# Kernel tuning notes

Hardware: AMD Instinct MI355X
Metric: run time of the kernel (lower is better)

The kernel has to match this reference:

```python
import jax, jax.numpy as jnp
import numpy as np

N_NODES = 150000
N_EDGES = 300000
N_LG_EDGES = 600000
N_TREE = 60000
HIDDEN = 256
DEPTH = 4
ATOM_FDIM = 35
BOND_FDIM = 5
NUM_GRAPHS = 2048


def setup_inputs() -> dict:
    key = jax.random.key(0)
    ks = jax.random.split(key, 14)
    return {
        "node_x": jax.random.normal(ks[0], (N_NODES, ATOM_FDIM), dtype=jnp.float32),
        "bond_x": jax.random.normal(ks[1], (N_EDGES, BOND_FDIM), dtype=jnp.float32),
        "tree_mess": jax.random.normal(ks[2], (N_TREE, HIDDEN), dtype=jnp.float32),
        "W_i": jax.random.normal(ks[3], (ATOM_FDIM + BOND_FDIM, HIDDEN), dtype=jnp.float32) * 0.05,
        "W_h": jax.random.normal(ks[4], (HIDDEN, HIDDEN), dtype=jnp.float32) * 0.05,
        "W_o": jax.random.normal(ks[5], (ATOM_FDIM + HIDDEN, HIDDEN), dtype=jnp.float32) * 0.05,
        "b_o": jax.random.normal(ks[6], (HIDDEN,), dtype=jnp.float32) * 0.05,
        "edge_src": jax.random.randint(ks[7], (N_EDGES,), 0, N_NODES, dtype=jnp.int64 if jax.config.jax_enable_x64 else jnp.int32).astype(jnp.int32),
        "edge_dst": jax.random.randint(ks[8], (N_EDGES,), 0, N_NODES).astype(jnp.int32),
        "lg_src": jax.random.randint(ks[9], (N_LG_EDGES,), 0, N_EDGES).astype(jnp.int32),
        "lg_dst": jax.random.randint(ks[10], (N_LG_EDGES,), 0, N_EDGES).astype(jnp.int32),
        "tgt_nodes": jax.random.randint(ks[11], (N_TREE,), 0, N_NODES).astype(jnp.int32),
        "graph_ids": jnp.sort(jax.random.randint(ks[12], (N_NODES,), 0, NUM_GRAPHS)).astype(jnp.int32),
        "num_graphs": NUM_GRAPHS,
    }


def reference(node_x, bond_x, tree_mess, W_i, W_h, W_o, b_o,
              edge_src, edge_dst, lg_src, lg_dst, tgt_nodes, graph_ids, num_graphs):
    n_nodes = node_x.shape[0]
    n_edges = bond_x.shape[0]

    # msg_input = W_i([src_atom_x ; bond_x])  (no bias)
    features = jnp.concatenate([node_x[edge_src], bond_x], axis=1)  # [E, 40]
    msg_input = features @ W_i                                       # [E, H]
    msg = jax.nn.relu(msg_input)

    # tree-message alpha: scatter_add tree messages onto target atoms (non-PAPER branch)
    node_alpha = jnp.zeros((n_nodes, msg.shape[1]), msg.dtype).at[tgt_nodes].add(tree_mess)
    edge_alpha = node_alpha[edge_src]  # apply_edges: alpha = src['alpha']

    # loopy BP on the line graph: accum = sum of incoming line-graph messages
    def body(msg, _):
        accum = jax.ops.segment_sum(msg[lg_src], lg_dst, num_segments=n_edges)
        msg = jax.nn.relu(msg_input + (accum + edge_alpha) @ W_h)
        return msg, None

    msg, _ = jax.lax.scan(body, msg, None, length=DEPTH - 1)

    # gather: m[v] = sum of msg over incoming edges; h = relu(W_o([x ; m + alpha]) + b)
    m = jax.ops.segment_sum(msg, edge_dst, num_segments=n_nodes)
    h = jax.nn.relu(jnp.concatenate([node_x, m + node_alpha], axis=1) @ W_o + b_o)

    # mean_nodes per graph
    counts = jax.ops.segment_sum(jnp.ones((n_nodes,), h.dtype), graph_ids, num_segments=num_graphs)
    g_sum = jax.ops.segment_sum(h, graph_ids, num_segments=num_graphs)
    g_repr = g_sum / jnp.maximum(counts, 1.0)[:, None]
    return g_repr
```

## Files before the change

### kernel.cpp

```cpp
#include <hip/hip_runtime.h>
#include <stdint.h>

#define HID 256
#define CAP 16

typedef __attribute__((ext_vector_type(8))) short bf16x8;
typedef __attribute__((ext_vector_type(4))) float f32x4;
typedef __attribute__((ext_vector_type(2))) float f32x2;

__device__ __forceinline__ float bf2f(unsigned short u) {
    union { unsigned int i; float f; } v; v.i = ((unsigned int)u) << 16; return v.f;
}
__device__ __forceinline__ unsigned short f2bf(float f) {
    union { float f; unsigned int i; } v; v.f = f;
    unsigned int r = (v.i + 0x7fffu + ((v.i >> 16) & 1u)) >> 16;
    return (unsigned short)r;
}
__device__ __forceinline__ float fp82f_sw(unsigned char b) {
    unsigned int s = (unsigned int)(b & 0x80) << 24;
    int e = (b >> 3) & 0xF;
    int m = b & 7;
    float v;
    if (e) v = __uint_as_float(((unsigned int)(e + 120) << 23) | ((unsigned int)m << 20));
    else   v = (float)m * 0.001953125f;
    return __uint_as_float(__float_as_uint(v) | s);
}
__device__ __forceinline__ unsigned char f2fp8_sw(float x) {
    unsigned int bits = __float_as_uint(x);
    unsigned char s = (unsigned char)((bits >> 24) & 0x80);
    float ax = fabsf(x);
    if (!(ax >= 0.001953125f)) {
        int n = (int)rintf(ax * 512.f);
        return s | (unsigned char)n;
    }
    if (ax >= 448.f) return s | 0x7E;
    int ex; float mant = frexpf(ax, &ex);
    int e = ex + 6;
    if (e >= 1) {
        int q = (int)rintf(mant * 16.f);
        if (q == 16) { q = 8; ++e; }
        if (e > 15 || (e == 15 && q > 14)) return s | 0x7E;
        return s | (unsigned char)((e << 3) | (q - 8));
    } else {
        int n = (int)rintf(ax * 512.f);
        if (n >= 8) return s | 0x08;
        return s | (unsigned char)n;
    }
}
__device__ __forceinline__ unsigned char f2fp8(float x) {
#if __has_builtin(__builtin_amdgcn_cvt_pk_fp8_f32)
    return (unsigned char)(__builtin_amdgcn_cvt_pk_fp8_f32(x, x, 0, false) & 0xff);
#else
    return f2fp8_sw(x);
#endif
}
__device__ __forceinline__ f32x4 fp8x4_to_f32(unsigned int u) {
#if __has_builtin(__builtin_amdgcn_cvt_pk_f32_fp8)
    f32x2 a = __builtin_amdgcn_cvt_pk_f32_fp8(u, false);
    f32x2 b = __builtin_amdgcn_cvt_pk_f32_fp8(u, true);
    f32x4 r; r[0] = a.x; r[1] = a.y; r[2] = b.x; r[3] = b.y;
    return r;
#else
    f32x4 r;
    #pragma unroll
    for (int q = 0; q < 4; ++q) r[q] = fp82f_sw((u >> (8 * q)) & 0xff);
    return r;
#endif
}
__device__ __forceinline__ bf16x8 fp8x8_to_bf16x8(uint2 raw) {
#if __has_builtin(__builtin_amdgcn_cvt_pk_f32_fp8)
    f32x2 p0 = __builtin_amdgcn_cvt_pk_f32_fp8(raw.x, false);
    f32x2 p1 = __builtin_amdgcn_cvt_pk_f32_fp8(raw.x, true);
    f32x2 p2 = __builtin_amdgcn_cvt_pk_f32_fp8(raw.y, false);
    f32x2 p3 = __builtin_amdgcn_cvt_pk_f32_fp8(raw.y, true);
    union { unsigned int u[4]; bf16x8 v; } cv;
    cv.u[0] = (__float_as_uint(p0.x) >> 16) | (__float_as_uint(p0.y) & 0xffff0000u);
    cv.u[1] = (__float_as_uint(p1.x) >> 16) | (__float_as_uint(p1.y) & 0xffff0000u);
    cv.u[2] = (__float_as_uint(p2.x) >> 16) | (__float_as_uint(p2.y) & 0xffff0000u);
    cv.u[3] = (__float_as_uint(p3.x) >> 16) | (__float_as_uint(p3.y) & 0xffff0000u);
    return cv.v;
#else
    union { unsigned short u[8]; bf16x8 v; } cv;
    #pragma unroll
    for (int q = 0; q < 4; ++q) cv.u[q]     = f2bf(fp82f_sw((raw.x >> (8 * q)) & 0xff));
    #pragma unroll
    for (int q = 0; q < 4; ++q) cv.u[4 + q] = f2bf(fp82f_sw((raw.y >> (8 * q)) & 0xff));
    return cv.v;
#endif
}

__device__ __forceinline__ void llds16(const void* g, void* l) {
    __builtin_amdgcn_global_load_lds(
        (const __attribute__((address_space(1))) void*)g,
        (__attribute__((address_space(3))) void*)l, 16, 0, 0);
}


__global__ void k_zero_f(float* __restrict__ p, size_t n) {
    size_t i = (size_t)blockIdx.x * 256 + threadIdx.x;
    if (i < n) p[i] = 0.f;
}
__global__ void k_diag(float* __restrict__ out, float v) {
    if (blockIdx.x == 0 && threadIdx.x == 0) out[0] = v;
}

__global__ void k_init(int* __restrict__ cnt_lg, int E,
                       int* __restrict__ cnt_nd, int* __restrict__ cnt_t, int N,
                       int* __restrict__ gcnt, int* __restrict__ gstart, int G) {
    int i = blockIdx.x * 256 + threadIdx.x;
    if (i < E) cnt_lg[i] = 0;
    if (i < N) { cnt_nd[i] = 0; cnt_t[i] = 0; }
    if (i < G) { gcnt[i] = 0; gstart[i] = N; }
}

__global__ void k_alpha(const float* __restrict__ tm, const int* __restrict__ cnt,
                        const int* __restrict__ bkt, unsigned char* __restrict__ alpha, int N) {
    int wave = threadIdx.x >> 6, lane = threadIdx.x & 63;
    int v = blockIdx.x * 4 + wave;
    if (v >= N) return;
    int d = cnt[v]; if (d > CAP) d = CAP;
    f32x4 s = {0.f, 0.f, 0.f, 0.f};
    const int* bb = bkt + (size_t)v * CAP;
    for (int t = 0; t < d; ++t) {
        int r = bb[t];
        f32x4 x = *(const f32x4*)(tm + (size_t)r * HID + lane * 4);
        #pragma unroll
        for (int k = 0; k < 4; ++k) s[k] += x[k];
    }
    union { unsigned char b[4]; unsigned int u; } ov;
    #pragma unroll
    for (int k = 0; k < 4; ++k) ov.b[k] = f2fp8(s[k]);
    *(unsigned int*)(alpha + (size_t)v * HID + lane * 4) = ov.u;
}

__global__ void k_wt_i(const float* __restrict__ W, unsigned short* __restrict__ Wt) {
    int i = blockIdx.x * 256 + threadIdx.x;
    int n = i >> 6, k = i & 63;
    Wt[i] = f2bf((k < 40) ? W[k * HID + n] : 0.f);
}
__global__ void k_wt_hi(const float* __restrict__ Wh, const float* __restrict__ Wi,
                        unsigned short* __restrict__ Wt) {
    int i = blockIdx.x * 256 + threadIdx.x;
    int n = i / 320, k = i % 320;
    float v;
    if (k < 256) v = Wh[(size_t)k * HID + n];
    else if (k < 296) v = Wi[(size_t)(k - 256) * HID + n];
    else v = 0.f;
    Wt[i] = f2bf(v);
}
__global__ void k_wt_o(const float* __restrict__ W, unsigned short* __restrict__ Wt) {
    int i = blockIdx.x * 256 + threadIdx.x;
    int n = i / 320, k = i % 320;
    float v;
    if (k < 256) v = W[(size_t)(35 + k) * HID + n];
    else if (k < 291) v = W[(size_t)(k - 256) * HID + n];
    else v = 0.f;
    Wt[i] = f2bf(v);
}

__global__ void k_a1(const float* __restrict__ nx, const float* __restrict__ bx,
                     const int* __restrict__ esrc, unsigned char* __restrict__ A1, int E) {
    int i = blockIdx.x * 256 + threadIdx.x;
    if (i >= E * 64) return;
    int e = i >> 6, k = i & 63;
    float v = 0.f;
    if (k < 35) v = nx[(size_t)esrc[e] * 35 + k];
    else if (k < 40) v = bx[(size_t)e * 5 + (k - 35)];
    A1[i] = f2fp8(v);
}

__global__ void k_x1(const float* __restrict__ nx, unsigned char* __restrict__ X1, int N) {
    int i = blockIdx.x * 256 + threadIdx.x;
    if (i >= N * 64) return;
    int v = i >> 6, k = i & 63;
    X1[i] = f2fp8((k < 35) ? nx[(size_t)v * 35 + k] : 0.f);
}

__global__ void k_fill(const int* __restrict__ dst, const int* __restrict__ val,
                       int* __restrict__ cnt, int* __restrict__ bkt, int n, int useval) {
    int i = blockIdx.x * 256 + threadIdx.x;
    if (i >= n) return;
    int d = dst[i];
    int p = atomicAdd(&cnt[d], 1);
    if (p < CAP) bkt[(size_t)d * CAP + p] = useval ? val[i] : i;
}

__global__ void k_gfill(const int* __restrict__ gid, int* __restrict__ gstart,
                        int* __restrict__ gcnt, int N) {
    int i = blockIdx.x * 256 + threadIdx.x;
    if (i >= N) return;
    int g = gid[i];
    atomicAdd(&gcnt[g], 1);
    atomicMin(&gstart[g], i);
}

template<int K1, int KTOT, int EPI, bool PF8, bool QF8, bool OUTF8>
__global__ __launch_bounds__(256, 2)
void gemm4(const void* __restrict__ Ap, int lda1,
           const void* __restrict__ Aq, int lda2,
           const unsigned short* __restrict__ B, int M,
           void* __restrict__ out, const float* __restrict__ bias)
{
    constexpr int NKC = KTOT / 64;
    __shared__ unsigned char Als[128 * 128];
    __shared__ unsigned char Bls[256 * 128];
    const int tid  = threadIdx.x;
    const int lane = tid & 63;
    const int wid  = tid >> 6;
    const int wm = wid & 1, wn = wid >> 1;
    const int row0 = blockIdx.x * 128;
    const int l15  = lane & 15;
    const int quad = lane >> 4;

    f32x4 acc[4][8] = {};

    const int sA8_r = lane >> 2, sA8_c = lane & 3;
    const int s16_r = lane >> 3, s16_c = lane & 7;

    #pragma unroll
    for (int kc = 0; kc < NKC; ++kc) {
        const bool pPart = (kc * 64 < K1);
        const void* As = pPart ? Ap : Aq;
        const int  lda  = pPart ? lda1 : lda2;
        const int  kofs = pPart ? kc * 64 : kc * 64 - K1;
        const bool f8   = pPart ? PF8 : QF8;

        if (f8) {
            #pragma unroll
            for (int t = 0; t < 2; ++t) {
                int r = wid * 32 + t * 16 + sA8_r;
                int ar = row0 + r; if (ar > M - 1) ar = M - 1;
                int ck = sA8_c ^ (r & 3);
                const unsigned char* g = (const unsigned char*)As + (size_t)ar * lda + kofs + ck * 16;
                llds16(g, &Als[(wid * 32 + t * 16) * 64]);
            }
        } else {
            #pragma unroll
            for (int t = 0; t < 4; ++t) {
                int r = wid * 32 + t * 8 + s16_r;
                int ar = row0 + r; if (ar > M - 1) ar = M - 1;
                int ck = s16_c ^ (r & 7);
                const unsigned char* g = (const unsigned char*)As + ((size_t)ar * lda + kofs) * 2 + ck * 16;
                llds16(g, &Als[(wid * 32 + t * 8) * 128]);
            }
        }
        #pragma unroll
        for (int t = 0; t < 8; ++t) {
            int r = wid * 64 + t * 8 + s16_r;
            int ck = s16_c ^ (r & 7);
            const unsigned char* g = (const unsigned char*)B + ((size_t)r * KTOT + kc * 64) * 2 + ck * 16;
            llds16(g, &Bls[(wid * 64 + t * 8) * 128]);
        }
        __syncthreads();

        #pragma unroll
        for (int kk = 0; kk < 64; kk += 32) {
            bf16x8 af[4];
            #pragma unroll
            for (int i = 0; i < 4; ++i) {
                int arow = wm * 64 + i * 16 + l15;
                if (f8) {
                    int ck = (kk >> 4) + (quad >> 1);
                    uint2 raw = *(const uint2*)&Als[arow * 64 + ((ck ^ (arow & 3)) << 4) + ((quad & 1) << 3)];
                    af[i] = fp8x8_to_bf16x8(raw);
                } else {
                    int ck = (kk >> 3) + quad;
                    af[i] = *(const bf16x8*)&Als[arow * 128 + ((ck ^ (arow & 7)) << 4)];
                }
            }
            #pragma unroll
            for (int j = 0; j < 8; ++j) {
                int brow = wn * 128 + j * 16 + l15;
                int ck = (kk >> 3) + quad;
                bf16x8 bfr = *(const bf16x8*)&Bls[brow * 128 + ((ck ^ (brow & 7)) << 4)];
                #pragma unroll
                for (int i = 0; i < 4; ++i)
                    acc[i][j] = __builtin_amdgcn_mfma_f32_16x16x32_bf16(af[i], bfr, acc[i][j], 0, 0, 0);
            }
        }
        if (kc + 1 < NKC) __syncthreads();
    }

    #pragma unroll
    for (int i = 0; i < 4; ++i) {
        int rbase = row0 + wm * 64 + i * 16 + quad * 4;
        #pragma unroll
        for (int r = 0; r < 4; ++r) {
            int row = rbase + r;
            if (row >= M) continue;
            #pragma unroll
            for (int j = 0; j < 8; ++j) {
                int col = wn * 128 + j * 16 + l15;
                float v = acc[i][j][r];
                if (EPI == 1) v += bias[col];
                v = v > 0.f ? v : 0.f;
                if (OUTF8) ((unsigned char*)out)[(size_t)row * HID + col] = f2fp8(v);
                else       ((unsigned short*)out)[(size_t)row * HID + col] = f2bf(v);
            }
        }
    }
}


__global__ void k_accum(const unsigned char* __restrict__ msg, const unsigned char* __restrict__ alpha,
                        const int* __restrict__ esrc, const int* __restrict__ cnt,
                        const int* __restrict__ bkt, unsigned char* __restrict__ accum, int E)
{
    int wave = threadIdx.x >> 6;
    int lane = threadIdx.x & 63;
    int sub  = lane >> 5;
    int sl   = lane & 31;
    int e = blockIdx.x * 8 + wave * 2 + sub;
    if (e >= E) return;
    int c = sl * 8;
    int src = esrc[e];
    int d = cnt[e]; if (d > CAP) d = CAP;
    uint2 au = *(const uint2*)(alpha + (size_t)src * HID + c);
    f32x4 s0 = fp8x4_to_f32(au.x);
    f32x4 s1 = fp8x4_to_f32(au.y);
    const int* bb = bkt + (size_t)e * CAP;
    for (int base = 0; base < d; base += 4) {
        int4 bi = *(const int4*)(bb + base);
        int rem = d - base;
        int i0 = bi.x;
        int i1 = (rem > 1) ? bi.y : bi.x;
        int i2 = (rem > 2) ? bi.z : bi.x;
        int i3 = (rem > 3) ? bi.w : bi.x;
        uint2 m0 = *(const uint2*)(msg + (size_t)i0 * HID + c);
        uint2 m1 = *(const uint2*)(msg + (size_t)i1 * HID + c);
        uint2 m2 = *(const uint2*)(msg + (size_t)i2 * HID + c);
        uint2 m3 = *(const uint2*)(msg + (size_t)i3 * HID + c);
        {   f32x4 vx = fp8x4_to_f32(m0.x), vy = fp8x4_to_f32(m0.y);
            #pragma unroll
            for (int k = 0; k < 4; ++k) { s0[k] += vx[k]; s1[k] += vy[k]; } }
        if (rem > 1) { f32x4 vx = fp8x4_to_f32(m1.x), vy = fp8x4_to_f32(m1.y);
            #pragma unroll
            for (int k = 0; k < 4; ++k) { s0[k] += vx[k]; s1[k] += vy[k]; } }
        if (rem > 2) { f32x4 vx = fp8x4_to_f32(m2.x), vy = fp8x4_to_f32(m2.y);
            #pragma unroll
            for (int k = 0; k < 4; ++k) { s0[k] += vx[k]; s1[k] += vy[k]; } }
        if (rem > 3) { f32x4 vx = fp8x4_to_f32(m3.x), vy = fp8x4_to_f32(m3.y);
            #pragma unroll
            for (int k = 0; k < 4; ++k) { s0[k] += vx[k]; s1[k] += vy[k]; } }
    }
    union { unsigned char b[8]; uint2 u; } ov;
    #pragma unroll
    for (int k = 0; k < 4; ++k) { ov.b[k] = f2fp8(s0[k]); ov.b[4 + k] = f2fp8(s1[k]); }
    *(uint2*)(accum + (size_t)e * HID + c) = ov.u;
}

__global__ void k_mpa(const unsigned char* __restrict__ msg, const unsigned char* __restrict__ alpha,
                      const int* __restrict__ cnt, const int* __restrict__ bkt,
                      unsigned short* __restrict__ Mb, int N)
{
    int wave = threadIdx.x >> 6;
    int lane = threadIdx.x & 63;
    int sub  = lane >> 5;
    int sl   = lane & 31;
    int v = blockIdx.x * 8 + wave * 2 + sub;
    if (v >= N) return;
    int c = sl * 8;
    int d = cnt[v]; if (d > CAP) d = CAP;
    uint2 au = *(const uint2*)(alpha + (size_t)v * HID + c);
    f32x4 s0 = fp8x4_to_f32(au.x);
    f32x4 s1 = fp8x4_to_f32(au.y);
    const int* bb = bkt + (size_t)v * CAP;
    for (int base = 0; base < d; base += 4) {
        int4 bi = *(const int4*)(bb + base);
        int rem = d - base;
        int i0 = bi.x;
        int i1 = (rem > 1) ? bi.y : bi.x;
        int i2 = (rem > 2) ? bi.z : bi.x;
        int i3 = (rem > 3) ? bi.w : bi.x;
        uint2 m0 = *(const uint2*)(msg + (size_t)i0 * HID + c);
        uint2 m1 = *(const uint2*)(msg + (size_t)i1 * HID + c);
        uint2 m2 = *(const uint2*)(msg + (size_t)i2 * HID + c);
        uint2 m3 = *(const uint2*)(msg + (size_t)i3 * HID + c);
        {   f32x4 vx = fp8x4_to_f32(m0.x), vy = fp8x4_to_f32(m0.y);
            #pragma unroll
            for (int k = 0; k < 4; ++k) { s0[k] += vx[k]; s1[k] += vy[k]; } }
        if (rem > 1) { f32x4 vx = fp8x4_to_f32(m1.x), vy = fp8x4_to_f32(m1.y);
            #pragma unroll
            for (int k = 0; k < 4; ++k) { s0[k] += vx[k]; s1[k] += vy[k]; } }
        if (rem > 2) { f32x4 vx = fp8x4_to_f32(m2.x), vy = fp8x4_to_f32(m2.y);
            #pragma unroll
            for (int k = 0; k < 4; ++k) { s0[k] += vx[k]; s1[k] += vy[k]; } }
        if (rem > 3) { f32x4 vx = fp8x4_to_f32(m3.x), vy = fp8x4_to_f32(m3.y);
            #pragma unroll
            for (int k = 0; k < 4; ++k) { s0[k] += vx[k]; s1[k] += vy[k]; } }
    }
    union { unsigned short h[8]; uint4 u; } ov;
    #pragma unroll
    for (int k = 0; k < 4; ++k) { ov.h[k] = f2bf(s0[k]); ov.h[4 + k] = f2bf(s1[k]); }
    *(uint4*)(Mb + (size_t)v * HID + c) = ov.u;
}

__global__ void k_gmean(const unsigned short* __restrict__ h, const int* __restrict__ gstart,
                        const int* __restrict__ gcnt, float* __restrict__ out, int G) {
    int g = blockIdx.x;
    int c = threadIdx.x;
    int st = gstart[g], n = gcnt[g];
    float s = 0.f;
    for (int r = 0; r < n; ++r) s += bf2f(h[(size_t)(st + r) * HID + c]);
    out[(size_t)g * HID + c] = (n > 0) ? s / (float)n : 0.f;
}

extern "C" void kernel_launch(void* const* d_in, const int* in_sizes, int n_in,
                              void* d_out, int out_size, void* d_ws, size_t ws_size,
                              hipStream_t stream)
{
    const float* node_x    = (const float*)d_in[0];
    const float* bond_x    = (const float*)d_in[1];
    const float* tree_mess = (const float*)d_in[2];
    const float* W_i       = (const float*)d_in[3];
    const float* W_h       = (const float*)d_in[4];
    const float* W_o       = (const float*)d_in[5];
    const float* b_o       = (const float*)d_in[6];
    const int* edge_src    = (const int*)d_in[7];
    const int* edge_dst    = (const int*)d_in[8];
    const int* lg_src      = (const int*)d_in[9];
    const int* lg_dst      = (const int*)d_in[10];
    const int* tgt_nodes   = (const int*)d_in[11];
    const int* graph_ids   = (const int*)d_in[12];

    const int N = in_sizes[0] / 35;
    const int E = in_sizes[1] / 5;
    const int T = in_sizes[2] / HID;
    const int L = in_sizes[9];
    const int G = out_size / HID;

    auto rup = [](size_t b) { return (b + 255) & ~(size_t)255; };
    const size_t szAcc = (size_t)E * HID;
    const size_t szMsg = (size_t)E * HID;
    const size_t szMbN = (size_t)N * HID * 2;
    const size_t R_acc = rup(szAcc > szMbN ? szAcc : szMbN);
    const size_t R_msg = rup(szMsg > szMbN ? szMsg : szMbN);
    const size_t R_al  = rup((size_t)N * HID);
    const size_t R_a1  = rup((size_t)E * 64);
    const size_t need = R_acc + R_msg + R_al + R_a1
        + rup(256 * 64 * 2) + rup((size_t)256 * 320 * 2) * 2
        + rup((size_t)E * 4) + rup((size_t)E * CAP * 4)
        + rup((size_t)N * 4) + rup((size_t)N * CAP * 4)
        + rup((size_t)N * 4) + rup((size_t)N * CAP * 4)
        + rup((size_t)G * 4) * 2;

    if (need > ws_size) {
        k_zero_f<<<(out_size + 255) / 256, 256, 0, stream>>>((float*)d_out, (size_t)out_size);
        k_diag<<<1, 64, 0, stream>>>((float*)d_out, (float)(ws_size >> 20));
        return;
    }

    char* w = (char*)d_ws;
    auto alloc = [&](size_t bytes) { char* p = w; w += (bytes + 255) & ~(size_t)255; return p; };
    char* r_acc = (char*)alloc(R_acc);
    char* r_msg = (char*)alloc(R_msg);
    char* r_al  = (char*)alloc(R_al);
    char* r_a1  = (char*)alloc(R_a1);
    unsigned short* Wt_i  = (unsigned short*)alloc(256 * 64 * 2);
    unsigned short* Wt_hi = (unsigned short*)alloc((size_t)256 * 320 * 2);
    unsigned short* Wt_o  = (unsigned short*)alloc((size_t)256 * 320 * 2);
    int* cnt_lg = (int*)alloc((size_t)E * 4);
    int* bkt_lg = (int*)alloc((size_t)E * CAP * 4);
    int* cnt_nd = (int*)alloc((size_t)N * 4);
    int* bkt_nd = (int*)alloc((size_t)N * CAP * 4);
    int* cnt_t  = (int*)alloc((size_t)N * 4);
    int* bkt_t  = (int*)alloc((size_t)N * CAP * 4);
    int* gstart = (int*)alloc((size_t)G * 4);
    int* gcnt   = (int*)alloc((size_t)G * 4);

    unsigned char*  accum = (unsigned char*)r_acc;
    unsigned short* Mb    = (unsigned short*)r_acc;
    unsigned char*  msg   = (unsigned char*)r_msg;
    unsigned short* h     = (unsigned short*)r_msg;
    unsigned char*  alpha = (unsigned char*)r_al;
    unsigned char*  A1    = (unsigned char*)r_a1;
    unsigned char*  X1    = (unsigned char*)r_a1;

    k_init<<<(E + 255) / 256, 256, 0, stream>>>(cnt_lg, E, cnt_nd, cnt_t, N, gcnt, gstart, G);

    k_wt_i<<<64, 256, 0, stream>>>(W_i, Wt_i);
    k_wt_hi<<<320, 256, 0, stream>>>(W_h, W_i, Wt_hi);
    k_wt_o<<<320, 256, 0, stream>>>(W_o, Wt_o);
    k_fill<<<(L + 255) / 256, 256, 0, stream>>>(lg_dst, lg_src, cnt_lg, bkt_lg, L, 1);
    k_fill<<<(E + 255) / 256, 256, 0, stream>>>(edge_dst, (const int*)nullptr, cnt_nd, bkt_nd, E, 0);
    k_fill<<<(T + 255) / 256, 256, 0, stream>>>(tgt_nodes, (const int*)nullptr, cnt_t, bkt_t, T, 0);
    k_gfill<<<(N + 255) / 256, 256, 0, stream>>>(graph_ids, gstart, gcnt, N);
    k_alpha<<<(N + 3) / 4, 256, 0, stream>>>(tree_mess, cnt_t, bkt_t, alpha, N);
    k_a1<<<(E * 64 + 255) / 256, 256, 0, stream>>>(node_x, bond_x, edge_src, A1, E);

    dim3 gE((E + 127) / 128, 1), gN((N + 127) / 128, 1);

    gemm4<0, 64, 0, false, true, true><<<gE, 256, 0, stream>>>(nullptr, 0, A1, 64, Wt_i, E, msg, nullptr);

    for (int it = 0; it < 3; ++it) {
        k_accum<<<(E + 7) / 8, 256, 0, stream>>>(msg, alpha, edge_src, cnt_lg, bkt_lg, accum, E);
        gemm4<256, 320, 0, true, true, true><<<gE, 256, 0, stream>>>(accum, 256, A1, 64, Wt_hi, E, msg, nullptr);
    }

    k_x1<<<(N * 64 + 255) / 256, 256, 0, stream>>>(node_x, X1, N);
    k_mpa<<<(N + 7) / 8, 256, 0, stream>>>(msg, alpha, cnt_nd, bkt_nd, Mb, N);
    gemm4<256, 320, 1, false, true, false><<<gN, 256, 0, stream>>>(Mb, 256, X1, 64, Wt_o, N, h, b_o);
    k_gmean<<<G, 256, 0, stream>>>(h, gstart, gcnt, (float*)d_out, G);
}
```

Measured before the change: 897.3 us.

## Double-buffer GEMM LDS staging, split output GEMM columns, widen accum vectors

Result: faster. 868.7 us (-3.2%).

```diff
diff --git a/kernel.cpp b/kernel.cpp
--- a/kernel.cpp
+++ b/kernel.cpp
@@ -194,37 +194,41 @@
     atomicMin(&gstart[g], i);
 }
 
-template<int K1, int KTOT, int EPI, bool PF8, bool QF8, bool OUTF8>
+template<int BN, int K1, int KTOT, int EPI, bool PF8, bool QF8, bool OUTF8>
 __global__ __launch_bounds__(256, 2)
-void gemm4(const void* __restrict__ Ap, int lda1,
+void gemm5(const void* __restrict__ Ap, int lda1,
            const void* __restrict__ Aq, int lda2,
            const unsigned short* __restrict__ B, int M,
            void* __restrict__ out, const float* __restrict__ bias)
 {
     constexpr int NKC = KTOT / 64;
-    __shared__ unsigned char Als[128 * 128];
-    __shared__ unsigned char Bls[256 * 128];
+    constexpr int NB  = (NKC > 1) ? 2 : 1;
+    constexpr bool ABF = (K1 > 0 && !PF8) || (KTOT > K1 && !QF8);
+    constexpr int ASZ = ABF ? 128 * 128 : 128 * 64;
+    constexpr int BSZ = BN * 128;
+    constexpr int JN  = BN / 32;
+    __shared__ unsigned char Als[NB * ASZ];
+    __shared__ unsigned char Bls[NB * BSZ];
     const int tid  = threadIdx.x;
     const int lane = tid & 63;
     const int wid  = tid >> 6;
     const int wm = wid & 1, wn = wid >> 1;
     const int row0 = blockIdx.x * 128;
+    const int colb = blockIdx.y * BN;
     const int l15  = lane & 15;
     const int quad = lane >> 4;
 
-    f32x4 acc[4][8] = {};
+    f32x4 acc[4][JN] = {};
 
     const int sA8_r = lane >> 2, sA8_c = lane & 3;
     const int s16_r = lane >> 3, s16_c = lane & 7;
 
-    #pragma unroll
-    for (int kc = 0; kc < NKC; ++kc) {
+    auto stageA = [&](int kc, int bb) {
         const bool pPart = (kc * 64 < K1);
         const void* As = pPart ? Ap : Aq;
         const int  lda  = pPart ? lda1 : lda2;
         const int  kofs = pPart ? kc * 64 : kc * 64 - K1;
         const bool f8   = pPart ? PF8 : QF8;
-
         if (f8) {
             #pragma unroll
             for (int t = 0; t < 2; ++t) {
@@ -232,7 +236,7 @@
                 int ar = row0 + r; if (ar > M - 1) ar = M - 1;
                 int ck = sA8_c ^ (r & 3);
                 const unsigned char* g = (const unsigned char*)As + (size_t)ar * lda + kofs + ck * 16;
-                llds16(g, &Als[(wid * 32 + t * 16) * 64]);
+                llds16(g, &Als[bb + (wid * 32 + t * 16) * 64]);
             }
         } else {
             #pragma unroll
@@ -241,18 +245,29 @@
                 int ar = row0 + r; if (ar > M - 1) ar = M - 1;
                 int ck = s16_c ^ (r & 7);
                 const unsigned char* g = (const unsigned char*)As + ((size_t)ar * lda + kofs) * 2 + ck * 16;
-                llds16(g, &Als[(wid * 32 + t * 8) * 128]);
+                llds16(g, &Als[bb + (wid * 32 + t * 8) * 128]);
             }
         }
+    };
+    auto stageB = [&](int kc, int bb) {
         #pragma unroll
-        for (int t = 0; t < 8; ++t) {
-            int r = wid * 64 + t * 8 + s16_r;
+        for (int t = 0; t < BN / 32; ++t) {
+            int r = wid * (BN / 4) + t * 8 + s16_r;
             int ck = s16_c ^ (r & 7);
-            const unsigned char* g = (const unsigned char*)B + ((size_t)r * KTOT + kc * 64) * 2 + ck * 16;
-            llds16(g, &Bls[(wid * 64 + t * 8) * 128]);
+            const unsigned char* g = (const unsigned char*)B + ((size_t)(colb + r) * KTOT + kc * 64) * 2 + ck * 16;
+            llds16(g, &Bls[bb + (wid * (BN / 4) + t * 8) * 128]);
         }
+    };
+
+    stageA(0, 0);
+    stageB(0, 0);
+    int cur = 0;
+    #pragma unroll
+    for (int kc = 0; kc < NKC; ++kc) {
         __syncthreads();
-
+        if (kc + 1 < NKC) { stageA(kc + 1, (cur ^ 1) * ASZ); stageB(kc + 1, (cur ^ 1) * BSZ); }
+        const bool f8 = (kc * 64 < K1) ? PF8 : QF8;
+        const int abase = cur * ASZ, bbase = cur * BSZ;
         #pragma unroll
         for (int kk = 0; kk < 64; kk += 32) {
             bf16x8 af[4];
@@ -261,24 +276,24 @@
                 int arow = wm * 64 + i * 16 + l15;
                 if (f8) {
                     int ck = (kk >> 4) + (quad >> 1);
-                    uint2 raw = *(const uint2*)&Als[arow * 64 + ((ck ^ (arow & 3)) << 4) + ((quad & 1) << 3)];
+                    uint2 raw = *(const uint2*)&Als[abase + arow * 64 + ((ck ^ (arow & 3)) << 4) + ((quad & 1) << 3)];
                     af[i] = fp8x8_to_bf16x8(raw);
                 } else {
                     int ck = (kk >> 3) + quad;
-                    af[i] = *(const bf16x8*)&Als[arow * 128 + ((ck ^ (arow & 7)) << 4)];
+                    af[i] = *(const bf16x8*)&Als[abase + arow * 128 + ((ck ^ (arow & 7)) << 4)];
                 }
             }
             #pragma unroll
-            for (int j = 0; j < 8; ++j) {
-                int brow = wn * 128 + j * 16 + l15;
+            for (int j = 0; j < JN; ++j) {
+                int brow = wn * (BN / 2) + j * 16 + l15;
                 int ck = (kk >> 3) + quad;
-                bf16x8 bfr = *(const bf16x8*)&Bls[brow * 128 + ((ck ^ (brow & 7)) << 4)];
+                bf16x8 bfr = *(const bf16x8*)&Bls[bbase + brow * 128 + ((ck ^ (brow & 7)) << 4)];
                 #pragma unroll
                 for (int i = 0; i < 4; ++i)
                     acc[i][j] = __builtin_amdgcn_mfma_f32_16x16x32_bf16(af[i], bfr, acc[i][j], 0, 0, 0);
             }
         }
-        if (kc + 1 < NKC) __syncthreads();
+        cur ^= 1;
     }
 
     #pragma unroll
@@ -289,8 +304,8 @@
             int row = rbase + r;
             if (row >= M) continue;
             #pragma unroll
-            for (int j = 0; j < 8; ++j) {
-                int col = wn * 128 + j * 16 + l15;
+            for (int j = 0; j < JN; ++j) {
+                int col = colb + wn * (BN / 2) + j * 16 + l15;
                 float v = acc[i][j][r];
                 if (EPI == 1) v += bias[col];
                 v = v > 0.f ? v : 0.f;
@@ -306,18 +321,20 @@
                         const int* __restrict__ esrc, const int* __restrict__ cnt,
                         const int* __restrict__ bkt, unsigned char* __restrict__ accum, int E)
 {
-    int wave = threadIdx.x >> 6;
-    int lane = threadIdx.x & 63;
-    int sub  = lane >> 5;
-    int sl   = lane & 31;
-    int e = blockIdx.x * 8 + wave * 2 + sub;
+    int tid  = threadIdx.x;
+    int lane = tid & 63, wave = tid >> 6;
+    int sub  = lane >> 4;
+    int sl   = lane & 15;
+    int e = blockIdx.x * 16 + wave * 4 + sub;
     if (e >= E) return;
-    int c = sl * 8;
+    int c = sl * 16;
     int src = esrc[e];
     int d = cnt[e]; if (d > CAP) d = CAP;
-    uint2 au = *(const uint2*)(alpha + (size_t)src * HID + c);
+    uint4 au = *(const uint4*)(alpha + (size_t)src * HID + c);
     f32x4 s0 = fp8x4_to_f32(au.x);
     f32x4 s1 = fp8x4_to_f32(au.y);
+    f32x4 s2 = fp8x4_to_f32(au.z);
+    f32x4 s3 = fp8x4_to_f32(au.w);
     const int* bb = bkt + (size_t)e * CAP;
     for (int base = 0; base < d; base += 4) {
         int4 bi = *(const int4*)(bb + base);
@@ -326,27 +343,32 @@
         int i1 = (rem > 1) ? bi.y : bi.x;
         int i2 = (rem > 2) ? bi.z : bi.x;
         int i3 = (rem > 3) ? bi.w : bi.x;
-        uint2 m0 = *(const uint2*)(msg + (size_t)i0 * HID + c);
-        uint2 m1 = *(const uint2*)(msg + (size_t)i1 * HID + c);
-        uint2 m2 = *(const uint2*)(msg + (size_t)i2 * HID + c);
-        uint2 m3 = *(const uint2*)(msg + (size_t)i3 * HID + c);
-        {   f32x4 vx = fp8x4_to_f32(m0.x), vy = fp8x4_to_f32(m0.y);
-            #pragma unroll
-            for (int k = 0; k < 4; ++k) { s0[k] += vx[k]; s1[k] += vy[k]; } }
-        if (rem > 1) { f32x4 vx = fp8x4_to_f32(m1.x), vy = fp8x4_to_f32(m1.y);
-            #pragma unroll
-            for (int k = 0; k < 4; ++k) { s0[k] += vx[k]; s1[k] += vy[k]; } }
-        if (rem > 2) { f32x4 vx = fp8x4_to_f32(m2.x), vy = fp8x4_to_f32(m2.y);
-            #pragma unroll
-            for (int k = 0; k < 4; ++k) { s0[k] += vx[k]; s1[k] += vy[k]; } }
-        if (rem > 3) { f32x4 vx = fp8x4_to_f32(m3.x), vy = fp8x4_to_f32(m3.y);
-            #pragma unroll
-            for (int k = 0; k < 4; ++k) { s0[k] += vx[k]; s1[k] += vy[k]; } }
-    }
-    union { unsigned char b[8]; uint2 u; } ov;
-    #pragma unroll
-    for (int k = 0; k < 4; ++k) { ov.b[k] = f2fp8(s0[k]); ov.b[4 + k] = f2fp8(s1[k]); }
-    *(uint2*)(accum + (size_t)e * HID + c) = ov.u;
+        uint4 m0 = *(const uint4*)(msg + (size_t)i0 * HID + c);
+        uint4 m1 = *(const uint4*)(msg + (size_t)i1 * HID + c);
+        uint4 m2 = *(const uint4*)(msg + (size_t)i2 * HID + c);
+        uint4 m3 = *(const uint4*)(msg + (size_t)i3 * HID + c);
+        {   f32x4 a0 = fp8x4_to_f32(m0.x), a1 = fp8x4_to_f32(m0.y), a2 = fp8x4_to_f32(m0.z), a3 = fp8x4_to_f32(m0.w);
+            #pragma unroll
+            for (int k = 0; k < 4; ++k) { s0[k] += a0[k]; s1[k] += a1[k]; s2[k] += a2[k]; s3[k] += a3[k]; } }
+        if (rem > 1) { f32x4 a0 = fp8x4_to_f32(m1.x), a1 = fp8x4_to_f32(m1.y), a2 = fp8x4_to_f32(m1.z), a3 = fp8x4_to_f32(m1.w);
+            #pragma unroll
+            for (int k = 0; k < 4; ++k) { s0[k] += a0[k]; s1[k] += a1[k]; s2[k] += a2[k]; s3[k] += a3[k]; } }
+        if (rem > 2) { f32x4 a0 = fp8x4_to_f32(m2.x), a1 = fp8x4_to_f32(m2.y), a2 = fp8x4_to_f32(m2.z), a3 = fp8x4_to_f32(m2.w);
+            #pragma unroll
+            for (int k = 0; k < 4; ++k) { s0[k] += a0[k]; s1[k] += a1[k]; s2[k] += a2[k]; s3[k] += a3[k]; } }
+        if (rem > 3) { f32x4 a0 = fp8x4_to_f32(m3.x), a1 = fp8x4_to_f32(m3.y), a2 = fp8x4_to_f32(m3.z), a3 = fp8x4_to_f32(m3.w);
+            #pragma unroll
+            for (int k = 0; k < 4; ++k) { s0[k] += a0[k]; s1[k] += a1[k]; s2[k] += a2[k]; s3[k] += a3[k]; } }
+    }
+    union { unsigned char b[16]; uint4 u; } ov;
+    #pragma unroll
+    for (int k = 0; k < 4; ++k) {
+        ov.b[k]      = f2fp8(s0[k]);
+        ov.b[4 + k]  = f2fp8(s1[k]);
+        ov.b[8 + k]  = f2fp8(s2[k]);
+        ov.b[12 + k] = f2fp8(s3[k]);
+    }
+    *(uint4*)(accum + (size_t)e * HID + c) = ov.u;
 }
 
 __global__ void k_mpa(const unsigned char* __restrict__ msg, const unsigned char* __restrict__ alpha,
@@ -488,17 +510,17 @@
     k_alpha<<<(N + 3) / 4, 256, 0, stream>>>(tree_mess, cnt_t, bkt_t, alpha, N);
     k_a1<<<(E * 64 + 255) / 256, 256, 0, stream>>>(node_x, bond_x, edge_src, A1, E);
 
-    dim3 gE((E + 127) / 128, 1), gN((N + 127) / 128, 1);
-
-    gemm4<0, 64, 0, false, true, true><<<gE, 256, 0, stream>>>(nullptr, 0, A1, 64, Wt_i, E, msg, nullptr);
+    dim3 gE((E + 127) / 128, 1), gN((N + 127) / 128, 2);
+
+    gemm5<256, 0, 64, 0, false, true, true><<<gE, 256, 0, stream>>>(nullptr, 0, A1, 64, Wt_i, E, msg, nullptr);
 
     for (int it = 0; it < 3; ++it) {
-        k_accum<<<(E + 7) / 8, 256, 0, stream>>>(msg, alpha, edge_src, cnt_lg, bkt_lg, accum, E);
-        gemm4<256, 320, 0, true, true, true><<<gE, 256, 0, stream>>>(accum, 256, A1, 64, Wt_hi, E, msg, nullptr);
+        k_accum<<<(E + 15) / 16, 256, 0, stream>>>(msg, alpha, edge_src, cnt_lg, bkt_lg, accum, E);
+        gemm5<256, 256, 320, 0, true, true, true><<<gE, 256, 0, stream>>>(accum, 256, A1, 64, Wt_hi, E, msg, nullptr);
     }
 
     k_x1<<<(N * 64 + 255) / 256, 256, 0, stream>>>(node_x, X1, N);
     k_mpa<<<(N + 7) / 8, 256, 0, stream>>>(msg, alpha, cnt_nd, bkt_nd, Mb, N);
-    gemm4<256, 320, 1, false, true, false><<<gN, 256, 0, stream>>>(Mb, 256, X1, 64, Wt_o, N, h, b_o);
+    gemm5<128, 256, 320, 1, false, true, false><<<gN, 256, 0, stream>>>(Mb, 256, X1, 64, Wt_o, N, h, b_o);
     k_gmean<<<G, 256, 0, stream>>>(h, gstart, gcnt, (float*)d_out, G);
 }
```

## Fuse line-graph message gather into the W_h GEMM prologue with ping-pong buffers

Applied to the files above, without the earlier changes.

After: 1.033 ms. +15.1%, slower.

```diff
diff --git a/kernel.cpp b/kernel.cpp
--- a/kernel.cpp
+++ b/kernel.cpp
@@ -194,15 +194,21 @@
     atomicMin(&gstart[g], i);
 }
 
-template<int K1, int KTOT, int EPI, bool PF8, bool QF8, bool OUTF8>
+template<int K1, int KTOT, int EPI, bool PF8, bool QF8, bool OUTF8, int FUSE, bool WHOLEK>
 __global__ __launch_bounds__(256, 2)
-void gemm4(const void* __restrict__ Ap, int lda1,
+void gemm7(const void* __restrict__ Ap, int lda1,
            const void* __restrict__ Aq, int lda2,
            const unsigned short* __restrict__ B, int M,
-           void* __restrict__ out, const float* __restrict__ bias)
+           void* __restrict__ out, const float* __restrict__ bias,
+           const unsigned char* __restrict__ g_alpha, const int* __restrict__ g_idx,
+           const int* __restrict__ g_cnt, const int* __restrict__ g_bkt)
 {
     constexpr int NKC = KTOT / 64;
-    __shared__ unsigned char Als[128 * 128];
+    constexpr int NK1 = K1 / 64;
+    constexpr int S1  = PF8 ? 8192 : 16384;
+    constexpr int S2  = QF8 ? 8192 : 16384;
+    constexpr int ATOT = WHOLEK ? (NK1 * S1 + (NKC - NK1) * S2) : (S1 > S2 ? S1 : S2);
+    __shared__ unsigned char Als[ATOT];
     __shared__ unsigned char Bls[256 * 128];
     const int tid  = threadIdx.x;
     const int lane = tid & 63;
@@ -217,14 +223,17 @@
     const int sA8_r = lane >> 2, sA8_c = lane & 3;
     const int s16_r = lane >> 3, s16_c = lane & 7;
 
-    #pragma unroll
-    for (int kc = 0; kc < NKC; ++kc) {
-        const bool pPart = (kc * 64 < K1);
+    auto aoff = [&](int kc) -> int {
+        if (!WHOLEK) return 0;
+        return (kc < NK1) ? kc * S1 : NK1 * S1 + (kc - NK1) * S2;
+    };
+
+    auto stageA_llds = [&](int kc, int dstoff) {
+        const bool pPart = (kc < NK1);
         const void* As = pPart ? Ap : Aq;
         const int  lda  = pPart ? lda1 : lda2;
-        const int  kofs = pPart ? kc * 64 : kc * 64 - K1;
+        const int  kofs = pPart ? kc * 64 : (kc - NK1) * 64;
         const bool f8   = pPart ? PF8 : QF8;
-
         if (f8) {
             #pragma unroll
             for (int t = 0; t < 2; ++t) {
@@ -232,7 +241,7 @@
                 int ar = row0 + r; if (ar > M - 1) ar = M - 1;
                 int ck = sA8_c ^ (r & 3);
                 const unsigned char* g = (const unsigned char*)As + (size_t)ar * lda + kofs + ck * 16;
-                llds16(g, &Als[(wid * 32 + t * 16) * 64]);
+                llds16(g, &Als[dstoff + (wid * 32 + t * 16) * 64]);
             }
         } else {
             #pragma unroll
@@ -241,9 +250,11 @@
                 int ar = row0 + r; if (ar > M - 1) ar = M - 1;
                 int ck = s16_c ^ (r & 7);
                 const unsigned char* g = (const unsigned char*)As + ((size_t)ar * lda + kofs) * 2 + ck * 16;
-                llds16(g, &Als[(wid * 32 + t * 8) * 128]);
+                llds16(g, &Als[dstoff + (wid * 32 + t * 8) * 128]);
             }
         }
+    };
+    auto stageB = [&](int kc) {
         #pragma unroll
         for (int t = 0; t < 8; ++t) {
             int r = wid * 64 + t * 8 + s16_r;
@@ -251,8 +262,56 @@
             const unsigned char* g = (const unsigned char*)B + ((size_t)r * KTOT + kc * 64) * 2 + ck * 16;
             llds16(g, &Bls[(wid * 64 + t * 8) * 128]);
         }
-        __syncthreads();
-
+    };
+
+    if (FUSE == 1) {
+        const unsigned char* msrc = (const unsigned char*)Ap;
+        const int grp = tid >> 4, sl = tid & 15;
+        #pragma unroll
+        for (int rr = 0; rr < 8; ++rr) {
+            int r = rr * 16 + grp;
+            int ar = row0 + r; if (ar > M - 1) ar = M - 1;
+            int src = g_idx[ar];
+            int d = g_cnt[ar]; if (d > CAP) d = CAP;
+            uint4 au = *(const uint4*)(g_alpha + (size_t)src * HID + sl * 16);
+            f32x4 s0 = fp8x4_to_f32(au.x);
+            f32x4 s1 = fp8x4_to_f32(au.y);
+            f32x4 s2 = fp8x4_to_f32(au.z);
+            f32x4 s3 = fp8x4_to_f32(au.w);
+            const int* bb = g_bkt + (size_t)ar * CAP;
+            for (int t = 0; t < d; ++t) {
+                uint4 mu = *(const uint4*)(msrc + (size_t)bb[t] * HID + sl * 16);
+                f32x4 a0 = fp8x4_to_f32(mu.x), a1 = fp8x4_to_f32(mu.y);
+                f32x4 a2 = fp8x4_to_f32(mu.z), a3 = fp8x4_to_f32(mu.w);
+                #pragma unroll
+                for (int k = 0; k < 4; ++k) { s0[k] += a0[k]; s1[k] += a1[k]; s2[k] += a2[k]; s3[k] += a3[k]; }
+            }
+            union { unsigned char b[16]; uint4 u; } ov;
+            #pragma unroll
+            for (int k = 0; k < 4; ++k) {
+                ov.b[k]      = f2fp8(s0[k]);
+                ov.b[4 + k]  = f2fp8(s1[k]);
+                ov.b[8 + k]  = f2fp8(s2[k]);
+                ov.b[12 + k] = f2fp8(s3[k]);
+            }
+            int seg = sl >> 2, ck = (sl & 3) ^ (r & 3);
+            *(uint4*)&Als[seg * 8192 + r * 64 + ck * 16] = ov.u;
+        }
+        #pragma unroll
+        for (int kc = NK1; kc < NKC; ++kc) stageA_llds(kc, aoff(kc));
+    } else if (WHOLEK) {
+        #pragma unroll
+        for (int kc = 0; kc < NKC; ++kc) stageA_llds(kc, aoff(kc));
+    } else {
+        stageA_llds(0, 0);
+    }
+    stageB(0);
+    __syncthreads();
+
+    #pragma unroll
+    for (int kc = 0; kc < NKC; ++kc) {
+        const bool f8  = (kc < NK1) ? PF8 : QF8;
+        const int ab = aoff(kc);
         #pragma unroll
         for (int kk = 0; kk < 64; kk += 32) {
             bf16x8 af[4];
@@ -261,11 +320,11 @@
                 int arow = wm * 64 + i * 16 + l15;
                 if (f8) {
                     int ck = (kk >> 4) + (quad >> 1);
-                    uint2 raw = *(const uint2*)&Als[arow * 64 + ((ck ^ (arow & 3)) << 4) + ((quad & 1) << 3)];
+                    uint2 raw = *(const uint2*)&Als[ab + arow * 64 + ((ck ^ (arow & 3)) << 4) + ((quad & 1) << 3)];
                     af[i] = fp8x8_to_bf16x8(raw);
                 } else {
                     int ck = (kk >> 3) + quad;
-                    af[i] = *(const bf16x8*)&Als[arow * 128 + ((ck ^ (arow & 7)) << 4)];
+                    af[i] = *(const bf16x8*)&Als[ab + arow * 128 + ((ck ^ (arow & 7)) << 4)];
                 }
             }
             #pragma unroll
@@ -278,7 +337,12 @@
                     acc[i][j] = __builtin_amdgcn_mfma_f32_16x16x32_bf16(af[i], bfr, acc[i][j], 0, 0, 0);
             }
         }
-        if (kc + 1 < NKC) __syncthreads();
+        if (kc + 1 < NKC) {
+            __syncthreads();
+            if (!WHOLEK) stageA_llds(kc + 1, 0);
+            stageB(kc + 1);
+            __syncthreads();
+        }
     }
 
     #pragma unroll
@@ -301,53 +365,6 @@
     }
 }
 
-
-__global__ void k_accum(const unsigned char* __restrict__ msg, const unsigned char* __restrict__ alpha,
-                        const int* __restrict__ esrc, const int* __restrict__ cnt,
-                        const int* __restrict__ bkt, unsigned char* __restrict__ accum, int E)
-{
-    int wave = threadIdx.x >> 6;
-    int lane = threadIdx.x & 63;
-    int sub  = lane >> 5;
-    int sl   = lane & 31;
-    int e = blockIdx.x * 8 + wave * 2 + sub;
-    if (e >= E) return;
-    int c = sl * 8;
-    int src = esrc[e];
-    int d = cnt[e]; if (d > CAP) d = CAP;
-    uint2 au = *(const uint2*)(alpha + (size_t)src * HID + c);
-    f32x4 s0 = fp8x4_to_f32(au.x);
-    f32x4 s1 = fp8x4_to_f32(au.y);
-    const int* bb = bkt + (size_t)e * CAP;
-    for (int base = 0; base < d; base += 4) {
-        int4 bi = *(const int4*)(bb + base);
-        int rem = d - base;
-        int i0 = bi.x;
-        int i1 = (rem > 1) ? bi.y : bi.x;
-        int i2 = (rem > 2) ? bi.z : bi.x;
-        int i3 = (rem > 3) ? bi.w : bi.x;
-        uint2 m0 = *(const uint2*)(msg + (size_t)i0 * HID + c);
-        uint2 m1 = *(const uint2*)(msg + (size_t)i1 * HID + c);
-        uint2 m2 = *(const uint2*)(msg + (size_t)i2 * HID + c);
-        uint2 m3 = *(const uint2*)(msg + (size_t)i3 * HID + c);
-        {   f32x4 vx = fp8x4_to_f32(m0.x), vy = fp8x4_to_f32(m0.y);
-            #pragma unroll
-            for (int k = 0; k < 4; ++k) { s0[k] += vx[k]; s1[k] += vy[k]; } }
-        if (rem > 1) { f32x4 vx = fp8x4_to_f32(m1.x), vy = fp8x4_to_f32(m1.y);
-            #pragma unroll
-            for (int k = 0; k < 4; ++k) { s0[k] += vx[k]; s1[k] += vy[k]; } }
-        if (rem > 2) { f32x4 vx = fp8x4_to_f32(m2.x), vy = fp8x4_to_f32(m2.y);
-            #pragma unroll
-            for (int k = 0; k < 4; ++k) { s0[k] += vx[k]; s1[k] += vy[k]; } }
-        if (rem > 3) { f32x4 vx = fp8x4_to_f32(m3.x), vy = fp8x4_to_f32(m3.y);
-            #pragma unroll
-            for (int k = 0; k < 4; ++k) { s0[k] += vx[k]; s1[k] += vy[k]; } }
-    }
-    union { unsigned char b[8]; uint2 u; } ov;
-    #pragma unroll
-    for (int k = 0; k < 4; ++k) { ov.b[k] = f2fp8(s0[k]); ov.b[4 + k] = f2fp8(s1[k]); }
-    *(uint2*)(accum + (size_t)e * HID + c) = ov.u;
-}
 
 __global__ void k_mpa(const unsigned char* __restrict__ msg, const unsigned char* __restrict__ alpha,
                       const int* __restrict__ cnt, const int* __restrict__ bkt,
@@ -468,9 +485,9 @@
     int* gstart = (int*)alloc((size_t)G * 4);
     int* gcnt   = (int*)alloc((size_t)G * 4);
 
-    unsigned char*  accum = (unsigned char*)r_acc;
+    unsigned char*  msgB  = (unsigned char*)r_acc;
     unsigned short* Mb    = (unsigned short*)r_acc;
-    unsigned char*  msg   = (unsigned char*)r_msg;
+    unsigned char*  msgA  = (unsigned char*)r_msg;
     unsigned short* h     = (unsigned short*)r_msg;
     unsigned char*  alpha = (unsigned char*)r_al;
     unsigned char*  A1    = (unsigned char*)r_a1;
@@ -490,15 +507,19 @@
 
     dim3 gE((E + 127) / 128, 1), gN((N + 127) / 128, 1);
 
-    gemm4<0, 64, 0, false, true, true><<<gE, 256, 0, stream>>>(nullptr, 0, A1, 64, Wt_i, E, msg, nullptr);
+    gemm7<0, 64, 0, false, true, true, 0, true><<<gE, 256, 0, stream>>>(
+        nullptr, 0, A1, 64, Wt_i, E, msgB, nullptr, nullptr, nullptr, nullptr, nullptr);
 
     for (int it = 0; it < 3; ++it) {
-        k_accum<<<(E + 7) / 8, 256, 0, stream>>>(msg, alpha, edge_src, cnt_lg, bkt_lg, accum, E);
-        gemm4<256, 320, 0, true, true, true><<<gE, 256, 0, stream>>>(accum, 256, A1, 64, Wt_hi, E, msg, nullptr);
+        const unsigned char* src = (it & 1) ? msgA : msgB;
+        unsigned char*       dst = (it & 1) ? msgB : msgA;
+        gemm7<256, 320, 0, true, true, true, 1, true><<<gE, 256, 0, stream>>>(
+            src, 256, A1, 64, Wt_hi, E, dst, nullptr, alpha, edge_src, cnt_lg, bkt_lg);
     }
 
     k_x1<<<(N * 64 + 255) / 256, 256, 0, stream>>>(node_x, X1, N);
-    k_mpa<<<(N + 7) / 8, 256, 0, stream>>>(msg, alpha, cnt_nd, bkt_nd, Mb, N);
-    gemm4<256, 320, 1, false, true, false><<<gN, 256, 0, stream>>>(Mb, 256, X1, 64, Wt_o, N, h, b_o);
+    k_mpa<<<(N + 7) / 8, 256, 0, stream>>>(msgA, alpha, cnt_nd, bkt_nd, Mb, N);
+    gemm7<256, 320, 1, false, true, false, 0, false><<<gN, 256, 0, stream>>>(
+        Mb, 256, X1, 64, Wt_o, N, h, b_o, nullptr, nullptr, nullptr, nullptr);
     k_gmean<<<G, 256, 0, stream>>>(h, gstart, gcnt, (float*)d_out, G);
 }
```
